# Performance work log

Hardware: AMD Instinct MI355X
Metric: run time of the kernel (lower is better)

Reference implementation:

```python
import jax, jax.numpy as jnp
import numpy as np

N, E, F_IN, H, D, HID, G = 50000, 800000, 64, 4, 32, 128, 1024
NEG_SLOPE = 0.2


def setup_inputs():
    key = jax.random.key(0)
    ks = jax.random.split(key, 32)
    inp = {
        "x": jax.random.normal(ks[0], (N, F_IN), dtype=jnp.float32),
        "edge_index": jax.random.randint(ks[1], (2, E), 0, N, dtype=jnp.int64),
        "batch": jnp.sort(jax.random.randint(ks[2], (N,), 0, G, dtype=jnp.int64)),
    }
    dims = [F_IN, HID, HID]
    i = 3
    for l, din in enumerate(dims):
        s = 1.0 / np.sqrt(din)
        inp[f"Wl{l}"] = jax.random.normal(ks[i], (din, H * D), dtype=jnp.float32) * s; i += 1
        inp[f"bl{l}"] = jnp.zeros((H * D,), dtype=jnp.float32)
        inp[f"Wr{l}"] = jax.random.normal(ks[i], (din, H * D), dtype=jnp.float32) * s; i += 1
        inp[f"br{l}"] = jnp.zeros((H * D,), dtype=jnp.float32)
        inp[f"att{l}"] = jax.random.normal(ks[i], (H, D), dtype=jnp.float32) * (1.0 / np.sqrt(D)); i += 1
        inp[f"b{l}"] = jnp.zeros((H * D,), dtype=jnp.float32)
    inp["Wh"] = jax.random.normal(ks[i], (HID, 1), dtype=jnp.float32) * (1.0 / np.sqrt(HID))
    inp["bh"] = jnp.zeros((1,), dtype=jnp.float32)
    return inp


def gatv2_layer(x, src, dst, Wl, bl, Wr, br, att, b):
    # GATv2Conv (eval mode, no dropout): e_ij = att . leaky_relu(Wl x_j + Wr x_i)
    xl = (x @ Wl + bl).reshape(-1, H, D)   # source transform
    xr = (x @ Wr + br).reshape(-1, H, D)   # target transform
    m = xl[src] + xr[dst]                  # [E,H,D]
    e = jnp.where(m >= 0, m, NEG_SLOPE * m)
    score = jnp.einsum("ehd,hd->eh", e, att)          # [E,H]
    smax = jax.ops.segment_max(score, dst, num_segments=N)  # [N,H]
    expv = jnp.exp(score - smax[dst])
    denom = jax.ops.segment_sum(expv, dst, num_segments=N)
    alpha = expv / denom[dst]                          # softmax over in-edges of dst
    agg = jax.ops.segment_sum(alpha[:, :, None] * xl[src], dst, num_segments=N)
    return agg.reshape(-1, H * D) + b


def reference(x, edge_index, batch, Wl0, bl0, Wr0, br0, att0, b0,
              Wl1, bl1, Wr1, br1, att1, b1,
              Wl2, bl2, Wr2, br2, att2, b2, Wh, bh):
    src, dst = edge_index[0], edge_index[1]
    params = [(Wl0, bl0, Wr0, br0, att0, b0),
              (Wl1, bl1, Wr1, br1, att1, b1),
              (Wl2, bl2, Wr2, br2, att2, b2)]
    h = x
    for p in params:
        h = gatv2_layer(h, src, dst, *p)
        h = jax.nn.elu(h)  # dropout inactive in eval
    # global mean pool over graphs
    sums = jax.ops.segment_sum(h, batch, num_segments=G)
    cnt = jax.ops.segment_sum(jnp.ones((h.shape[0],), h.dtype), batch, num_segments=G)
    pooled = sums / jnp.maximum(cnt, 1.0)[:, None]
    return pooled @ Wh + bh
```

## Files before the change

kernel.cpp:

```cpp
#include <hip/hip_runtime.h>
#include <math.h>

#define N_NODES 50000
#define N_EDGES 800000
#define HD 128
#define GG 1024
#define NEG_SLOPE 0.2f
#define SCAN_B 1024
#define NB ((N_NODES + SCAN_B - 1) / SCAN_B)
#define NXCONV (N_NODES * 64)
#define NWCONV 81920

typedef __attribute__((ext_vector_type(8))) short bf16x8;
typedef __attribute__((ext_vector_type(4))) float f32x4;
typedef __attribute__((ext_vector_type(2))) float f32x2;

__device__ __forceinline__ unsigned short f2bf(float v) {
    unsigned u = __float_as_uint(v);
    u += 0x7fff + ((u >> 16) & 1);
    return (unsigned short)(u >> 16);
}
__device__ __forceinline__ float bf2f(unsigned short s) {
    return __uint_as_float((unsigned)s << 16);
}

__global__ void convert_prep(const float* __restrict__ x,
                             unsigned short* __restrict__ Xh, unsigned short* __restrict__ Xl,
                             const float* __restrict__ W0l, const float* __restrict__ W0r,
                             const float* __restrict__ W1l, const float* __restrict__ W1r,
                             const float* __restrict__ W2l, const float* __restrict__ W2r,
                             unsigned short* __restrict__ Wth, unsigned short* __restrict__ Wtl,
                             const int* __restrict__ dst, int* __restrict__ deg,
                             const int* __restrict__ batch, int* __restrict__ gptr)
{
    const int i = blockIdx.x * 256 + threadIdx.x;
    if (i < NXCONV) {
        const float v = x[i];
        const unsigned short hi = f2bf(v);
        Xh[i] = hi;
        Xl[i] = f2bf(v - bf2f(hi));
        return;
    }
    if (i < NXCONV + NWCONV) {
        const int t = i - NXCONV;
        const float* Wl; const float* Wr;
        int c, k, o;
        if (t < 16384) {
            c = t >> 6; k = t & 63; o = t;
            Wl = W0l; Wr = W0r;
        } else if (t < 49152) {
            const int b = t - 16384; c = b >> 7; k = b & 127; o = 32768 + b;
            Wl = W1l; Wr = W1r;
        } else {
            const int b = t - 49152; c = b >> 7; k = b & 127; o = 65536 + b;
            Wl = W2l; Wr = W2r;
        }
        const float v = (c < 128) ? Wl[(size_t)k * 128 + c] : Wr[(size_t)k * 128 + (c - 128)];
        const unsigned short hi = f2bf(v);
        Wth[o] = hi;
        Wtl[o] = f2bf(v - bf2f(hi));
        return;
    }
    const int e = i - NXCONV - NWCONV;
    if (e < N_EDGES) atomicAdd(&deg[dst[e]], 1);
    if (e > N_NODES) return;
    if (e == 0) {
        for (int g = 0; g <= batch[0]; g++) gptr[g] = 0;
    } else if (e == N_NODES) {
        for (int g = batch[N_NODES - 1] + 1; g <= GG; g++) gptr[g] = N_NODES;
    } else {
        const int b0 = batch[e - 1], b1 = batch[e];
        for (int g = b0 + 1; g <= b1; g++) gptr[g] = e;
    }
}

__launch_bounds__(SCAN_B)
__global__ void scan_block(const int* __restrict__ deg, int* __restrict__ rowptr,
                           int* __restrict__ btot)
{
    __shared__ int s[SCAN_B];
    const int tid = threadIdx.x;
    const int i = blockIdx.x * SCAN_B + tid;
    int v = (i < N_NODES) ? deg[i] : 0;
    s[tid] = v;
    __syncthreads();
    for (int off = 1; off < SCAN_B; off <<= 1) {
        int t = (tid >= off) ? s[tid - off] : 0;
        __syncthreads();
        s[tid] += t;
        __syncthreads();
    }
    if (i < N_NODES) rowptr[i] = s[tid] - v;
    if (tid == SCAN_B - 1) btot[blockIdx.x] = s[SCAN_B - 1];
}

__launch_bounds__(256)
__global__ void scan_add(const int* __restrict__ btot, int* __restrict__ rowptr,
                         int* __restrict__ cursor)
{
    __shared__ int sb[NB + 1];
    const int tid = threadIdx.x;
    if (tid < 64) {
        const int v = (tid < NB) ? btot[tid] : 0;
        int incl = v;
        #pragma unroll
        for (int off = 1; off < 64; off <<= 1) {
            const int t = __shfl_up(incl, off);
            if (tid >= off) incl += t;
        }
        if (tid < NB) sb[tid] = incl - v;
        if (tid == NB - 1) sb[NB] = incl;
    }
    __syncthreads();
    const int i = blockIdx.x * 256 + tid;
    if (i < N_NODES) {
        const int r = rowptr[i] + sb[i >> 10];
        rowptr[i] = r;
        cursor[i] = r;
    }
    if (i == N_NODES) rowptr[N_NODES] = sb[NB];
}

__global__ void scatter_csr(const int* __restrict__ src, const int* __restrict__ dst,
                            int* __restrict__ cursor, int* __restrict__ csr_src)
{
    int e = blockIdx.x * 256 + threadIdx.x;
    if (e >= N_EDGES) return;
    int pos = atomicAdd(&cursor[dst[e]], 1);
    csr_src[pos] = src[e];
}

template<int K>
__launch_bounds__(256)
__global__ void gemm_lds(const unsigned short* __restrict__ Xh, const unsigned short* __restrict__ Xl,
                         const unsigned short* __restrict__ Wth, const unsigned short* __restrict__ Wtl,
                         const float* __restrict__ bl, const float* __restrict__ br,
                         float* __restrict__ Cl, float* __restrict__ Cr, int n)
{
    constexpr int NCH = K / 32;
    constexpr int STR = K + 8;
    constexpr int RT  = (N_NODES + 63) / 64;
    __shared__ unsigned short AsH[64 * STR], AsL[64 * STR];
    const int tid  = threadIdx.x;
    const int wave = tid >> 6;
    const int lane = tid & 63;
    const int quad = lane >> 4;
    const int l15  = lane & 15;
    const int cg   = blockIdx.x & 1;
    const int rs   = blockIdx.x >> 1;
    const int NS   = gridDim.x >> 1;
    const int colid = cg * 4 + wave;
    const int cb32  = colid * 32;

    bf16x8 Bh[NCH][2], Bo[NCH][2];
    #pragma unroll
    for (int ch = 0; ch < NCH; ch++)
        #pragma unroll
        for (int nt = 0; nt < 2; nt++) {
            const size_t wo = (size_t)(cb32 + nt * 16 + l15) * K + ch * 32 + quad * 8;
            Bh[ch][nt] = *(const bf16x8*)(Wth + wo);
            Bo[ch][nt] = *(const bf16x8*)(Wtl + wo);
        }

    const int cb = cb32 & 127;
    const float* bias = (colid < 4) ? bl : br;
    float* C = (colid < 4) ? Cl : Cr;
    const float bv0 = bias[cb + l15];
    const float bv1 = bias[cb + 16 + l15];

    for (int rt = rs; rt < RT; rt += NS) {
        const int row0 = rt * 64;
        {
            constexpr int THR = K / 8;
            constexpr int RPP = 256 / THR;
            const int sr = tid / THR, seg = tid % THR;
            #pragma unroll
            for (int ps = 0; ps < 64 / RPP; ps++) {
                const int r = ps * RPP + sr;
                int gr = row0 + r;
                gr = (gr < n) ? gr : (n - 1);
                const size_t go = (size_t)gr * K + seg * 8;
                *(uint4*)&AsH[r * STR + seg * 8] = *(const uint4*)(Xh + go);
                *(uint4*)&AsL[r * STR + seg * 8] = *(const uint4*)(Xl + go);
            }
        }
        __syncthreads();

        f32x4 acc[4][2];
        #pragma unroll
        for (int mt = 0; mt < 4; mt++) {
            acc[mt][0] = (f32x4){0.f, 0.f, 0.f, 0.f};
            acc[mt][1] = (f32x4){0.f, 0.f, 0.f, 0.f};
        }
        #pragma unroll
        for (int ch = 0; ch < NCH; ch++) {
            bf16x8 ah[4], al[4];
            #pragma unroll
            for (int mt = 0; mt < 4; mt++) {
                ah[mt] = *(const bf16x8*)&AsH[(mt * 16 + l15) * STR + ch * 32 + quad * 8];
                al[mt] = *(const bf16x8*)&AsL[(mt * 16 + l15) * STR + ch * 32 + quad * 8];
            }
            #pragma unroll
            for (int nt = 0; nt < 2; nt++)
                #pragma unroll
                for (int mt = 0; mt < 4; mt++) {
                    acc[mt][nt] = __builtin_amdgcn_mfma_f32_16x16x32_bf16(ah[mt], Bh[ch][nt], acc[mt][nt], 0, 0, 0);
                    acc[mt][nt] = __builtin_amdgcn_mfma_f32_16x16x32_bf16(ah[mt], Bo[ch][nt], acc[mt][nt], 0, 0, 0);
                    acc[mt][nt] = __builtin_amdgcn_mfma_f32_16x16x32_bf16(al[mt], Bh[ch][nt], acc[mt][nt], 0, 0, 0);
                }
        }

        #pragma unroll
        for (int nt = 0; nt < 2; nt++) {
            const float bv = nt ? bv1 : bv0;
            #pragma unroll
            for (int mt = 0; mt < 4; mt++)
                #pragma unroll
                for (int r = 0; r < 4; r++) {
                    const int row = row0 + mt * 16 + quad * 4 + r;
                    if (row < n)
                        C[(size_t)row * 128 + cb + nt * 16 + l15] = acc[mt][nt][r] + bv;
                }
        }
        __syncthreads();
    }
}

template<int LAST>
__launch_bounds__(256)
__global__ void node_attn(const float* __restrict__ xl, const float* __restrict__ xr,
                          const int* __restrict__ rowptr, const int* __restrict__ csr_src,
                          const float* __restrict__ att, const float* __restrict__ bvec,
                          unsigned short* __restrict__ Hh, unsigned short* __restrict__ Hl,
                          const float* __restrict__ Wh, float* __restrict__ pernode)
{
    const int node = (blockIdx.x * 256 + threadIdx.x) >> 6;
    const int lane = threadIdx.x & 63;
    if (node >= N_NODES) return;
    const int grp = lane >> 4;
    const int li  = lane & 15;

    const size_t nb = (size_t)node * HD + li * 8;
    f32x2 xrp[4], awp[4];
    {
        const float4 a = *(const float4*)(xr + nb);
        const float4 b = *(const float4*)(xr + nb + 4);
        xrp[0] = (f32x2){a.x, a.y}; xrp[1] = (f32x2){a.z, a.w};
        xrp[2] = (f32x2){b.x, b.y}; xrp[3] = (f32x2){b.z, b.w};
        const float4 c = *(const float4*)(att + li * 8);
        const float4 d = *(const float4*)(att + li * 8 + 4);
        awp[0] = (f32x2){c.x, c.y}; awp[1] = (f32x2){c.z, c.w};
        awp[2] = (f32x2){d.x, d.y}; awp[3] = (f32x2){d.z, d.w};
    }
    const f32x2 nsl = (f32x2){NEG_SLOPE, NEG_SLOPE};
    const int beg = rowptr[node];
    const int end = rowptr[node + 1];

    float m = -1e30f, l = 0.f;
    f32x2 accp[4];
    #pragma unroll
    for (int j = 0; j < 4; j++) accp[j] = (f32x2){0.f, 0.f};

    f32x2 vp[4];
    {
        const int e0 = beg + grp;
        const int s0 = (e0 < end) ? csr_src[e0] : 0;
        const float4 a = *(const float4*)(xl + (size_t)s0 * HD + li * 8);
        const float4 b = *(const float4*)(xl + (size_t)s0 * HD + li * 8 + 4);
        vp[0] = (f32x2){a.x, a.y}; vp[1] = (f32x2){a.z, a.w};
        vp[2] = (f32x2){b.x, b.y}; vp[3] = (f32x2){b.z, b.w};
    }

    for (int base = beg; base < end; base += 4) {
        const bool valid = (base + grp) < end;
        f32x2 np[4];
        #pragma unroll
        for (int j = 0; j < 4; j++) np[j] = vp[j];
        if (base + 4 < end) {
            const int e2 = base + 4 + grp;
            const int s2 = (e2 < end) ? csr_src[e2] : 0;
            const float4 a = *(const float4*)(xl + (size_t)s2 * HD + li * 8);
            const float4 b = *(const float4*)(xl + (size_t)s2 * HD + li * 8 + 4);
            np[0] = (f32x2){a.x, a.y}; np[1] = (f32x2){a.z, a.w};
            np[2] = (f32x2){b.x, b.y}; np[3] = (f32x2){b.z, b.w};
        }
        f32x2 pd0 = (f32x2){0.f, 0.f}, pd1 = (f32x2){0.f, 0.f};
        #pragma unroll
        for (int j = 0; j < 4; j++) {
            f32x2 t = vp[j] + xrp[j];
            const f32x2 u = t * nsl;
            t[0] = fmaxf(t[0], u[0]);
            t[1] = fmaxf(t[1], u[1]);
            if (j & 1) pd1 = t * awp[j] + pd1;
            else       pd0 = t * awp[j] + pd0;
        }
        const f32x2 pds = pd0 + pd1;
        float p = pds[0] + pds[1];
        p += __shfl_xor(p, 1);
        p += __shfl_xor(p, 2);

        const float mn = valid ? fmaxf(m, p) : m;
        const float w  = valid ? __expf(p - mn) : 0.f;
        const float sc = __expf(m - mn);
        l = fmaf(l, sc, w);
        const f32x2 w2  = (f32x2){w, w};
        const f32x2 sc2 = (f32x2){sc, sc};
        #pragma unroll
        for (int j = 0; j < 4; j++) {
            accp[j] = accp[j] * sc2 + w2 * vp[j];
            vp[j] = np[j];
        }
        m = mn;
    }

    #pragma unroll
    for (int off = 16; off < 64; off <<= 1) {
        const float mo = __shfl_xor(m, off);
        const float lo = __shfl_xor(l, off);
        f32x2 bo[4];
        #pragma unroll
        for (int j = 0; j < 4; j++) {
            bo[j][0] = __shfl_xor(accp[j][0], off);
            bo[j][1] = __shfl_xor(accp[j][1], off);
        }
        const float mm = fmaxf(m, mo);
        const float e1 = __expf(m - mm);
        const float e2 = __expf(mo - mm);
        l = l * e1 + lo * e2;
        const f32x2 e1p = (f32x2){e1, e1};
        const f32x2 e2p = (f32x2){e2, e2};
        #pragma unroll
        for (int j = 0; j < 4; j++)
            accp[j] = accp[j] * e1p + bo[j] * e2p;
        m = mm;
    }

    if (grp == 0) {
        const float inv = (l > 0.f) ? 1.f / l : 0.f;
        const float4 bb0 = *(const float4*)(bvec + li * 8);
        const float4 bb1 = *(const float4*)(bvec + li * 8 + 4);
        float o[8];
        o[0] = fmaf(accp[0][0], inv, bb0.x);
        o[1] = fmaf(accp[0][1], inv, bb0.y);
        o[2] = fmaf(accp[1][0], inv, bb0.z);
        o[3] = fmaf(accp[1][1], inv, bb0.w);
        o[4] = fmaf(accp[2][0], inv, bb1.x);
        o[5] = fmaf(accp[2][1], inv, bb1.y);
        o[6] = fmaf(accp[3][0], inv, bb1.z);
        o[7] = fmaf(accp[3][1], inv, bb1.w);
        #pragma unroll
        for (int j = 0; j < 8; j++)
            o[j] = (o[j] > 0.f) ? o[j] : expm1f(o[j]);
        if (LAST) {
            const float4 w0 = *(const float4*)(Wh + li * 8);
            const float4 w1 = *(const float4*)(Wh + li * 8 + 4);
            float da = o[0] * w0.x + o[2] * w0.z;
            float db = o[1] * w0.y + o[3] * w0.w;
            da = fmaf(o[4], w1.x, da); db = fmaf(o[5], w1.y, db);
            da = fmaf(o[6], w1.z, da); db = fmaf(o[7], w1.w, db);
            float d = da + db;
            d += __shfl_xor(d, 1);
            d += __shfl_xor(d, 2);
            d += __shfl_xor(d, 4);
            d += __shfl_xor(d, 8);
            if (li == 0) pernode[node] = d;
        } else {
            bf16x8 hv, lv;
            #pragma unroll
            for (int j = 0; j < 8; j++) {
                unsigned short h = f2bf(o[j]);
                hv[j] = (short)h;
                lv[j] = (short)f2bf(o[j] - bf2f(h));
            }
            *(bf16x8*)(Hh + nb) = hv;
            *(bf16x8*)(Hl + nb) = lv;
        }
    }
}

__launch_bounds__(256)
__global__ void finish_head(const float* __restrict__ pernode, const int* __restrict__ gptr,
                            const float* __restrict__ bh, float* __restrict__ out)
{
    const int g = (blockIdx.x * 256 + threadIdx.x) >> 6;
    const int lane = threadIdx.x & 63;
    if (g >= GG) return;
    const int b0 = gptr[g], b1 = gptr[g + 1];
    float s = 0.f;
    for (int i = b0 + lane; i < b1; i += 64) s += pernode[i];
    s += __shfl_xor(s, 1);
    s += __shfl_xor(s, 2);
    s += __shfl_xor(s, 4);
    s += __shfl_xor(s, 8);
    s += __shfl_xor(s, 16);
    s += __shfl_xor(s, 32);
    if (lane == 0) out[g] = s / fmaxf((float)(b1 - b0), 1.f) + bh[0];
}

extern "C" void kernel_launch(void* const* d_in, const int* in_sizes, int n_in,
                              void* d_out, int out_size, void* d_ws, size_t ws_size,
                              hipStream_t stream)
{
    const float* x     = (const float*)d_in[0];
    const int*   edge  = (const int*)d_in[1];
    const int*   batch = (const int*)d_in[2];
    const int*   src   = edge;
    const int*   dst   = edge + N_EDGES;
    const float* Wh    = (const float*)d_in[21];
    const float* bh    = (const float*)d_in[22];
    float* out = (float*)d_out;

    const size_t N128 = (size_t)N_NODES * HD;
    float* buf_xl = (float*)d_ws;
    float* buf_xr = buf_xl + N128;
    unsigned short* Xh  = (unsigned short*)(buf_xr + N128);
    unsigned short* Xl_ = Xh + N128;
    unsigned short* Wth = Xl_ + N128;
    unsigned short* Wtl = Wth + 3 * 256 * 128;
    int* deg       = (int*)(Wtl + 3 * 256 * 128);
    float* pernode = (float*)(deg + N_NODES);
    int* rowptr  = (int*)(pernode + N_NODES);
    int* cursor  = rowptr + N_NODES + 1;
    int* csr_src = cursor + N_NODES;
    int* btot    = csr_src + N_EDGES;
    int* gptr    = btot + NB;

    hipMemsetAsync(deg, 0, (size_t)N_NODES * sizeof(int), stream);
    convert_prep<<<(NXCONV + NWCONV + N_EDGES + 255) / 256, 256, 0, stream>>>(
        x, Xh, Xl_,
        (const float*)d_in[3], (const float*)d_in[5],
        (const float*)d_in[9], (const float*)d_in[11],
        (const float*)d_in[15], (const float*)d_in[17],
        Wth, Wtl, dst, deg, batch, gptr);
    scan_block<<<NB, SCAN_B, 0, stream>>>(deg, rowptr, btot);
    scan_add<<<(N_NODES + 256) / 256, 256, 0, stream>>>(btot, rowptr, cursor);
    scatter_csr<<<(N_EDGES + 255) / 256, 256, 0, stream>>>(src, dst, cursor, csr_src);

    const int gemm_grid = 512;
    const int attn_grid = (N_NODES + 3) / 4;

    for (int l = 0; l < 3; l++) {
        const float* bl  = (const float*)d_in[4 + 6 * l];
        const float* br  = (const float*)d_in[6 + 6 * l];
        const float* att = (const float*)d_in[7 + 6 * l];
        const float* bb  = (const float*)d_in[8 + 6 * l];

        if (l == 0)
            gemm_lds<64><<<gemm_grid, 256, 0, stream>>>(Xh, Xl_, Wth, Wtl,
                                                        bl, br, buf_xl, buf_xr, N_NODES);
        else
            gemm_lds<128><<<gemm_grid, 256, 0, stream>>>(Xh, Xl_,
                                                         Wth + l * 256 * 128, Wtl + l * 256 * 128,
                                                         bl, br, buf_xl, buf_xr, N_NODES);
        if (l < 2)
            node_attn<0><<<attn_grid, 256, 0, stream>>>(buf_xl, buf_xr, rowptr, csr_src,
                                                        att, bb, Xh, Xl_,
                                                        nullptr, nullptr);
        else
            node_attn<1><<<attn_grid, 256, 0, stream>>>(buf_xl, buf_xr, rowptr, csr_src,
                                                        att, bb, nullptr, nullptr,
                                                        Wh, pernode);
    }

    finish_head<<<GG / 4, 256, 0, stream>>>(pernode, gptr, bh, out);
}
```

Measured before the change: 445.2 us.

## Sort CSR neighbor lists per row and vectorize input bf16 split conversion

```diff
diff --git a/kernel.cpp b/kernel.cpp
--- a/kernel.cpp
+++ b/kernel.cpp
@@ -1,5 +1,6 @@
 #include <hip/hip_runtime.h>
 #include <math.h>
+#include <limits.h>
 
 #define N_NODES 50000
 #define N_EDGES 800000
@@ -8,7 +9,7 @@
 #define NEG_SLOPE 0.2f
 #define SCAN_B 1024
 #define NB ((N_NODES + SCAN_B - 1) / SCAN_B)
-#define NXCONV (N_NODES * 64)
+#define NXV4 800000
 #define NWCONV 81920
 
 typedef __attribute__((ext_vector_type(8))) short bf16x8;
@@ -34,15 +35,19 @@
                              const int* __restrict__ batch, int* __restrict__ gptr)
 {
     const int i = blockIdx.x * 256 + threadIdx.x;
-    if (i < NXCONV) {
-        const float v = x[i];
-        const unsigned short hi = f2bf(v);
-        Xh[i] = hi;
-        Xl[i] = f2bf(v - bf2f(hi));
+    if (i < NXV4) {
+        const float4 v = *(const float4*)(x + (size_t)i * 4);
+        ushort4 h, lo;
+        h.x = f2bf(v.x); lo.x = f2bf(v.x - bf2f(h.x));
+        h.y = f2bf(v.y); lo.y = f2bf(v.y - bf2f(h.y));
+        h.z = f2bf(v.z); lo.z = f2bf(v.z - bf2f(h.z));
+        h.w = f2bf(v.w); lo.w = f2bf(v.w - bf2f(h.w));
+        *(ushort4*)(Xh + (size_t)i * 4) = h;
+        *(ushort4*)(Xl + (size_t)i * 4) = lo;
         return;
     }
-    if (i < NXCONV + NWCONV) {
-        const int t = i - NXCONV;
+    if (i < NXV4 + NWCONV) {
+        const int t = i - NXV4;
         const float* Wl; const float* Wr;
         int c, k, o;
         if (t < 16384) {
@@ -61,7 +66,7 @@
         Wtl[o] = f2bf(v - bf2f(hi));
         return;
     }
-    const int e = i - NXCONV - NWCONV;
+    const int e = i - NXV4 - NWCONV;
     if (e < N_EDGES) atomicAdd(&deg[dst[e]], 1);
     if (e > N_NODES) return;
     if (e == 0) {
@@ -128,6 +133,29 @@
     if (e >= N_EDGES) return;
     int pos = atomicAdd(&cursor[dst[e]], 1);
     csr_src[pos] = src[e];
+}
+
+__launch_bounds__(256)
+__global__ void sort_rows(const int* __restrict__ rowptr, int* __restrict__ csr_src)
+{
+    const int node = (blockIdx.x * 256 + threadIdx.x) >> 6;
+    const int lane = threadIdx.x & 63;
+    if (node >= N_NODES) return;
+    const int b = rowptr[node], e = rowptr[node + 1];
+    const int d = e - b;
+    if (d <= 1 || d > 64) return;
+    int v = (lane < d) ? csr_src[b + lane] : INT_MAX;
+    #pragma unroll
+    for (int k = 2; k <= 64; k <<= 1) {
+        #pragma unroll
+        for (int j = k >> 1; j > 0; j >>= 1) {
+            const int partner = __shfl_xor(v, j);
+            const bool up = ((lane & k) == 0);
+            const bool keepmin = (((lane & j) == 0) == up);
+            v = keepmin ? min(v, partner) : max(v, partner);
+        }
+    }
+    if (lane < d) csr_src[b + lane] = v;
 }
 
 template<int K>
@@ -426,7 +454,7 @@
     int* gptr    = btot + NB;
 
     hipMemsetAsync(deg, 0, (size_t)N_NODES * sizeof(int), stream);
-    convert_prep<<<(NXCONV + NWCONV + N_EDGES + 255) / 256, 256, 0, stream>>>(
+    convert_prep<<<(NXV4 + NWCONV + N_EDGES + 256) / 256, 256, 0, stream>>>(
         x, Xh, Xl_,
         (const float*)d_in[3], (const float*)d_in[5],
         (const float*)d_in[9], (const float*)d_in[11],
@@ -435,6 +463,7 @@
     scan_block<<<NB, SCAN_B, 0, stream>>>(deg, rowptr, btot);
     scan_add<<<(N_NODES + 256) / 256, 256, 0, stream>>>(btot, rowptr, cursor);
     scatter_csr<<<(N_EDGES + 255) / 256, 256, 0, stream>>>(src, dst, cursor, csr_src);
+    sort_rows<<<(N_NODES + 3) / 4, 256, 0, stream>>>(rowptr, csr_src);
 
     const int gemm_grid = 512;
     const int attn_grid = (N_NODES + 3) / 4;
```

Measured after the change: 454.2 us. 2.0% more time.
